# Optimization experiments

Measured on AMD Instinct MI355X. Metric: run time of the kernel, lower is better.

## Reference

```python
import jax, jax.numpy as jnp
import numpy as np

E, IN, OUT, T = 8, 4096, 4096, 8192
GS = IN  # groupsize=-1 -> groupsize = infeatures


def setup_inputs() -> dict:
    key = jax.random.key(0)
    k1, k2, k3, k4, k5 = jax.random.split(key, 5)
    x = jax.random.normal(k1, (T, IN), dtype=jnp.float16)
    indices = jax.random.randint(k2, (T,), 0, E, dtype=jnp.int32)
    # int32 words each packing 8 int4 nonzero values (2:4 sparse -> IN*OUT/2 values per expert)
    qweight = jax.random.randint(k3, (E, IN // 32, OUT * 16 // 8), 0, 2**31 - 1, dtype=jnp.int32)
    meta = jax.random.randint(k4, (E, OUT, IN // 16), 0, 2**15, dtype=jnp.int32).astype(jnp.int16)
    scales = (jax.random.uniform(k5, (E, IN // GS, OUT), dtype=jnp.float32) * 0.02 + 0.001).astype(jnp.float16)
    return {"x": x, "indices": indices, "qweight": qweight, "meta": meta, "scales": scales}


def _dequant_24(qweight, meta, scales):
    """Decode packed int4 + 2:4-sparsity metadata into dense fp32 weights (E, OUT, IN)."""
    # unpack 8 int4 nibbles per int32 word, symmetric zero-point 8
    nib = (qweight[..., None] >> (4 * jnp.arange(8, dtype=jnp.int32))) & 0xF  # (E, IN//32, 2*OUT, 8)
    vals = nib.reshape(E, IN // 2, OUT).transpose(0, 2, 1).astype(jnp.float32) - 8.0  # (E, OUT, IN//2)
    m = meta.astype(jnp.int32) & 0xFFFF
    sub = (m[..., None] >> (2 * jnp.arange(8, dtype=jnp.int32))) & 0x3  # (E, OUT, IN//16, 8)
    grp = (jnp.arange(8, dtype=jnp.int32) // 2) * 4                      # group-of-4 base within 16-block
    base = 16 * jnp.arange(IN // 16, dtype=jnp.int32)                    # 16-block base
    dense_col = (base[None, None, :, None] + grp[None, None, None, :] + sub).reshape(E, OUT, IN // 2)
    eidx = jnp.arange(E)[:, None, None]
    oidx = jnp.arange(OUT)[None, :, None]
    W = jnp.zeros((E, OUT, IN), jnp.float32).at[eidx, oidx, dense_col].add(vals)
    # per-group dequant scales: (E, IN//GS, OUT) -> (E, OUT, IN)
    s = jnp.repeat(scales.astype(jnp.float32), GS, axis=1).transpose(0, 2, 1)
    return W * s


def reference(x, indices, qweight, meta, scales):
    W = _dequant_24(qweight, meta, scales)  # (E, OUT, IN)
    y = jnp.zeros((x.shape[0], OUT), jnp.float32)
    for e in range(E):  # fixed small expert count
        xe = jnp.where((indices == e)[:, None], x, 0).astype(jnp.float32)
        y = y + xe @ W[e].T
    return y.astype(x.dtype)
```

## Files before the change

kernel.cpp:

```cpp
#include <hip/hip_runtime.h>

#define E_N   8
#define IN_N  4096
#define OUT_N 4096
#define T_N   8192

#define BM 128
#define BN 256
#define BK 64
#define NTHREADS 512

typedef unsigned short u16;
typedef __bf16 bf16_t;
typedef bf16_t bf16x8 __attribute__((ext_vector_type(8)));
typedef u16    u16x8  __attribute__((ext_vector_type(8)));
typedef float  f32x4  __attribute__((ext_vector_type(4)));

#define GLOAD16(gsrc, ldst) \
    __builtin_amdgcn_global_load_lds( \
        (const __attribute__((address_space(1))) unsigned int*)(gsrc), \
        (__attribute__((address_space(3))) unsigned int*)(ldst), 16, 0, 0)

__device__ int g_cnt[E_N];
__device__ int g_base[E_N];
__device__ int g_ids[T_N];
__device__ int g_meta_wide;
__device__ u16 g_W[(long)E_N * OUT_N * IN_N];
__device__ u16 g_xb[(long)T_N * IN_N];

__device__ __forceinline__ u16 f2bf(float f) {
    unsigned u = __builtin_bit_cast(unsigned, f);
    u += 0x7FFFu + ((u >> 16) & 1u);
    return (u16)(u >> 16);
}

__global__ void sort_tokens(const int* __restrict__ idx, const u16* __restrict__ meta16) {
    __shared__ int cnt[E_N], off[E_N];
    __shared__ int probe;
    const int tid = threadIdx.x;
    if (tid == 0) probe = 0;
    if (tid < E_N) cnt[tid] = 0;
    __syncthreads();
    if (tid < 64) {
        unsigned v = meta16[2 * (tid * 131072) + 1];
        if (v) atomicOr(&probe, 1);
    }
    for (int t = tid; t < T_N; t += blockDim.x) atomicAdd(&cnt[idx[t] & 7], 1);
    __syncthreads();
    if (tid == 0) {
        int s = 0;
        for (int e = 0; e < E_N; ++e) { g_cnt[e] = cnt[e]; g_base[e] = s; off[e] = s; s += cnt[e]; }
        g_meta_wide = (probe == 0) ? 1 : 0;
    }
    __syncthreads();
    for (int t = tid; t < T_N; t += blockDim.x) {
        int p = atomicAdd(&off[idx[t] & 7], 1);
        if (p >= 0 && p < T_N) g_ids[p] = t;
    }
}

__global__ __launch_bounds__(256, 4)
void xb_convert(const float* __restrict__ x) {
    const int p = blockIdx.x;
    int tok = g_ids[p];
    if ((unsigned)tok >= (unsigned)T_N) tok = 0;
    const float* src = x + (long)tok * IN_N;
    u16* dst = g_xb + (long)p * IN_N;
    const int tid = threadIdx.x;
    float va[16];
    #pragma unroll
    for (int c4 = 0; c4 < 4; ++c4) {
        float4 v = *reinterpret_cast<const float4*>(src + tid * 16 + c4 * 4);
        va[c4 * 4 + 0] = v.x; va[c4 * 4 + 1] = v.y; va[c4 * 4 + 2] = v.z; va[c4 * 4 + 3] = v.w;
    }
    unsigned wp[8];
    #pragma unroll
    for (int p8 = 0; p8 < 8; ++p8)
        wp[p8] = (unsigned)f2bf(va[2 * p8]) | ((unsigned)f2bf(va[2 * p8 + 1]) << 16);
    *reinterpret_cast<int4*>(dst + tid * 16)     = make_int4((int)wp[0], (int)wp[1], (int)wp[2], (int)wp[3]);
    *reinterpret_cast<int4*>(dst + tid * 16 + 8) = make_int4((int)wp[4], (int)wp[5], (int)wp[6], (int)wp[7]);
}

__global__ __launch_bounds__(256, 4)
void decode_w(const int* __restrict__ qw, const void* __restrict__ meta) {
    const int e   = blockIdx.z;
    const int kt0 = blockIdx.y * 4;
    const int o   = blockIdx.x * 256 + threadIdx.x;
    const bool mwide = (g_meta_wide != 0);
    unsigned mws[16];
    if (mwide) {
        const int* mp = (const int*)meta + ((long)e * OUT_N + o) * (IN_N / 16) + kt0 * 4;
        #pragma unroll
        for (int i = 0; i < 16; ++i) mws[i] = (unsigned)mp[i] & 0xFFFFu;
    } else {
        const u16* mp = (const u16*)meta + ((long)e * OUT_N + o) * (IN_N / 16) + kt0 * 4;
        #pragma unroll
        for (int i = 0; i < 16; ++i) mws[i] = mp[i];
    }
    const unsigned sh = (o & 7) << 2;
    #pragma unroll
    for (int ki = 0; ki < 4; ++ki) {
        const int kt = kt0 + ki;
        unsigned wp[32];
        #pragma unroll
        for (int gi = 0; gi < 4; ++gi) {
            const int g = kt * 4 + gi;
            const unsigned mw = mws[ki * 4 + gi];
            const int* qp = qw + ((e * (IN_N / 32) + (g >> 1)) << 13) + (o >> 3) + ((g & 1) << 12);
            int d[16];
            #pragma unroll
            for (int p = 0; p < 16; ++p) d[p] = 0;
            #pragma unroll
            for (int grp = 0; grp < 4; ++grp) {
                const unsigned w0 = (unsigned)qp[(2 * grp) * 512];
                const unsigned w1 = (unsigned)qp[(2 * grp + 1) * 512];
                const int v0 = (int)((w0 >> sh) & 0xF) - 8;
                const int v1 = (int)((w1 >> sh) & 0xF) - 8;
                const int s0 = (mw >> (4 * grp)) & 3;
                const int s1 = (mw >> (4 * grp + 2)) & 3;
                #pragma unroll
                for (int q = 0; q < 4; ++q) {
                    int t0 = (s0 == q) ? v0 : 0;
                    int t1 = (s1 == q) ? v1 : 0;
                    d[grp * 4 + q] = t0 + t1;
                }
            }
            #pragma unroll
            for (int p = 0; p < 8; ++p) {
                unsigned lo = __builtin_bit_cast(unsigned, (float)d[2 * p])     >> 16;
                unsigned hi = __builtin_bit_cast(unsigned, (float)d[2 * p + 1]) >> 16;
                wp[gi * 8 + p] = lo | (hi << 16);
            }
        }
        u16* wr = g_W + ((long)(e * 64 + kt) * OUT_N + o) * 64;
        #pragma unroll
        for (int q4 = 0; q4 < 8; ++q4)
            *reinterpret_cast<int4*>(wr + q4 * 8) =
                make_int4((int)wp[q4 * 4], (int)wp[q4 * 4 + 1], (int)wp[q4 * 4 + 2], (int)wp[q4 * 4 + 3]);
    }
}

__global__ __launch_bounds__(NTHREADS, 1)
void moe_gemm(const float* __restrict__ scales, float* __restrict__ y) {
    const int e = blockIdx.z;
    int cnt = g_cnt[e];
    if (cnt < 0) cnt = 0;
    if (cnt > T_N) cnt = T_N;
    const int m0 = blockIdx.y * BM;
    if (m0 >= cnt) return;
    const int n0 = blockIdx.x * BN;
    int base = g_base[e];
    if (base < 0) base = 0;
    if (base > T_N - cnt) base = T_N - cnt;

    __shared__ __align__(16) u16 As[BM * BK];
    __shared__ __align__(16) u16 Bs[BN * BK];

    const int tid  = threadIdx.x;
    const int lane = tid & 63;
    const int wm   = (tid >> 6) >> 2;
    const int wn   = (tid >> 6) & 3;

    const int r0 = tid >> 3, kc = tid & 7;
    long ar0 = (long)base + m0 + r0;       if (ar0 > T_N - 1) ar0 = T_N - 1;
    long ar1 = (long)base + m0 + 64 + r0;  if (ar1 > T_N - 1) ar1 = T_N - 1;
    const u16* asrc0 = g_xb + ar0 * IN_N + kc * 8;
    const u16* asrc1 = g_xb + ar1 * IN_N + kc * 8;
    u16* adst0 = &As[tid * 8];
    u16* adst1 = &As[(tid + 512) * 8];
    const u16* bsrc = g_W + ((long)e * 64 * OUT_N + n0) * 64 + tid * 8;

    f32x4 acc[4][4];
    #pragma unroll
    for (int i = 0; i < 4; ++i)
        #pragma unroll
        for (int j = 0; j < 4; ++j) acc[i][j] = (f32x4){0.f, 0.f, 0.f, 0.f};

    for (int k0 = 0; k0 < IN_N; k0 += BK) {
        GLOAD16(asrc0 + k0, adst0);
        GLOAD16(asrc1 + k0, adst1);
        #pragma unroll
        for (int it = 0; it < 4; ++it)
            GLOAD16(bsrc + it * 4096, &Bs[(tid + it * 512) * 8]);
        bsrc += (long)OUT_N * 64;
        __syncthreads();
        #pragma unroll
        for (int kk = 0; kk < BK; kk += 32) {
            bf16x8 af[4], bfr[4];
            #pragma unroll
            for (int mf = 0; mf < 4; ++mf) {
                const int r = wm * 64 + mf * 16 + (lane & 15);
                u16x8 v = *reinterpret_cast<const u16x8*>(&As[r * 64 + kk + ((lane >> 4) << 3)]);
                af[mf] = __builtin_bit_cast(bf16x8, v);
            }
            #pragma unroll
            for (int nf = 0; nf < 4; ++nf) {
                const int r = wn * 64 + nf * 16 + (lane & 15);
                u16x8 v = *reinterpret_cast<const u16x8*>(&Bs[r * 64 + kk + ((lane >> 4) << 3)]);
                bfr[nf] = __builtin_bit_cast(bf16x8, v);
            }
            #pragma unroll
            for (int mf = 0; mf < 4; ++mf)
                #pragma unroll
                for (int nf = 0; nf < 4; ++nf)
                    acc[mf][nf] = __builtin_amdgcn_mfma_f32_16x16x32_bf16(af[mf], bfr[nf], acc[mf][nf], 0, 0, 0);
        }
        __syncthreads();
    }

    const int* toks = g_ids + base;
    float sc[4];
    #pragma unroll
    for (int nf = 0; nf < 4; ++nf)
        sc[nf] = scales[e * OUT_N + n0 + wn * 64 + nf * 16 + (lane & 15)];
    #pragma unroll
    for (int mf = 0; mf < 4; ++mf) {
        #pragma unroll
        for (int r = 0; r < 4; ++r) {
            const int row = m0 + wm * 64 + mf * 16 + ((lane >> 4) << 2) + r;
            if (row >= cnt) continue;
            int tok = toks[row];
            if ((unsigned)tok >= (unsigned)T_N) continue;
            float* yrow = y + (long)tok * OUT_N;
            #pragma unroll
            for (int nf = 0; nf < 4; ++nf) {
                const int col = n0 + wn * 64 + nf * 16 + (lane & 15);
                yrow[col] = acc[mf][nf][r] * sc[nf];
            }
        }
    }
}

extern "C" void kernel_launch(void* const* d_in, const int* in_sizes, int n_in,
                              void* d_out, int out_size, void* d_ws, size_t ws_size,
                              hipStream_t stream) {
    const float* x      = nullptr;
    const int* indices  = nullptr;
    const int* qw       = nullptr;
    const void* meta    = nullptr;
    const float* scales = nullptr;
    int big_seen = 0;
    for (int i = 0; i < n_in; ++i) {
        long s = in_sizes[i];
        if (s == 33554432L)      x = (const float*)d_in[i];
        else if (s == 8192L)     indices = (const int*)d_in[i];
        else if (s == 32768L)    scales = (const float*)d_in[i];
        else if (s == 8388608L) {
            if (big_seen++ == 0)  qw = (const int*)d_in[i];
            else                  meta = d_in[i];
        }
    }
    if (!x || !indices || !qw || !meta || !scales) return;
    float* y = (float*)d_out;

    hipLaunchKernelGGL(sort_tokens, dim3(1), dim3(1024), 0, stream, indices, (const u16*)meta);
    hipLaunchKernelGGL(xb_convert, dim3(T_N), dim3(256), 0, stream, x);
    hipLaunchKernelGGL(decode_w, dim3(OUT_N / 256, 16, E_N), dim3(256), 0, stream, qw, meta);
    hipLaunchKernelGGL(moe_gemm, dim3(OUT_N / BN, T_N / BM, E_N), dim3(NTHREADS), 0, stream, scales, y);
}
```

Before: 725.5 us.

## XOR-swizzle LDS tiles to remove bank conflicts; warp-aggregate token sort atomics

The A tile load now fetches 16-byte chunks from a column chosen by XORing with the row, so the LDS layout is swizzled. The decoded weight matrix is written to global memory in the same XOR-permuted chunk order, which lets the B tile keep its straight copy. The fragment reads apply the matching XOR, which should remove LDS bank conflicts on the row-strided 128-byte reads. Separately, the token sort replaces per-thread shared atomics with ballot/popcount warp aggregation, trading more instructions for fewer atomics in a tiny kernel.

```diff
diff --git a/kernel.cpp b/kernel.cpp
--- a/kernel.cpp
+++ b/kernel.cpp
@@ -38,6 +38,7 @@
     __shared__ int cnt[E_N], off[E_N];
     __shared__ int probe;
     const int tid = threadIdx.x;
+    const int lane = tid & 63;
     if (tid == 0) probe = 0;
     if (tid < E_N) cnt[tid] = 0;
     __syncthreads();
@@ -45,7 +46,15 @@
         unsigned v = meta16[2 * (tid * 131072) + 1];
         if (v) atomicOr(&probe, 1);
     }
-    for (int t = tid; t < T_N; t += blockDim.x) atomicAdd(&cnt[idx[t] & 7], 1);
+    for (int t0 = tid - lane; t0 < T_N; t0 += blockDim.x) {
+        const int t = t0 + lane;
+        const int my = idx[t] & 7;
+        #pragma unroll
+        for (int e = 0; e < E_N; ++e) {
+            unsigned long long m = __ballot(my == e);
+            if (lane == 0 && m) atomicAdd(&cnt[e], __popcll(m));
+        }
+    }
     __syncthreads();
     if (tid == 0) {
         int s = 0;
@@ -53,9 +62,22 @@
         g_meta_wide = (probe == 0) ? 1 : 0;
     }
     __syncthreads();
-    for (int t = tid; t < T_N; t += blockDim.x) {
-        int p = atomicAdd(&off[idx[t] & 7], 1);
-        if (p >= 0 && p < T_N) g_ids[p] = t;
+    for (int t0 = tid - lane; t0 < T_N; t0 += blockDim.x) {
+        const int t = t0 + lane;
+        const int my = idx[t] & 7;
+        #pragma unroll
+        for (int e = 0; e < E_N; ++e) {
+            unsigned long long m = __ballot(my == e);
+            if (my == e) {
+                int below = __popcll(m & ((1ull << lane) - 1ull));
+                int basep = 0;
+                if (below == 0) basep = atomicAdd(&off[e], __popcll(m));
+                int src = __ffsll((long long)m) - 1;
+                basep = __shfl(basep, src);
+                int p = basep + below;
+                if (p >= 0 && p < T_N) g_ids[p] = t;
+            }
+        }
     }
 }
 
@@ -98,6 +120,7 @@
         for (int i = 0; i < 16; ++i) mws[i] = mp[i];
     }
     const unsigned sh = (o & 7) << 2;
+    const int osw = o & 7;
     #pragma unroll
     for (int ki = 0; ki < 4; ++ki) {
         const int kt = kt0 + ki;
@@ -134,9 +157,9 @@
         }
         u16* wr = g_W + ((long)(e * 64 + kt) * OUT_N + o) * 64;
         #pragma unroll
-        for (int q4 = 0; q4 < 8; ++q4)
-            *reinterpret_cast<int4*>(wr + q4 * 8) =
-                make_int4((int)wp[q4 * 4], (int)wp[q4 * 4 + 1], (int)wp[q4 * 4 + 2], (int)wp[q4 * 4 + 3]);
+        for (int h = 0; h < 8; ++h)
+            *reinterpret_cast<int4*>(wr + (h ^ osw) * 8) =
+                make_int4((int)wp[h * 4], (int)wp[h * 4 + 1], (int)wp[h * 4 + 2], (int)wp[h * 4 + 3]);
     }
 }
 
@@ -161,11 +184,12 @@
     const int wm   = (tid >> 6) >> 2;
     const int wn   = (tid >> 6) & 3;
 
-    const int r0 = tid >> 3, kc = tid & 7;
+    const int r0 = tid >> 3;
+    const int kc_swz = (tid & 7) ^ (r0 & 7);
     long ar0 = (long)base + m0 + r0;       if (ar0 > T_N - 1) ar0 = T_N - 1;
     long ar1 = (long)base + m0 + 64 + r0;  if (ar1 > T_N - 1) ar1 = T_N - 1;
-    const u16* asrc0 = g_xb + ar0 * IN_N + kc * 8;
-    const u16* asrc1 = g_xb + ar1 * IN_N + kc * 8;
+    const u16* asrc0 = g_xb + ar0 * IN_N + kc_swz * 8;
+    const u16* asrc1 = g_xb + ar1 * IN_N + kc_swz * 8;
     u16* adst0 = &As[tid * 8];
     u16* adst1 = &As[(tid + 512) * 8];
     const u16* bsrc = g_W + ((long)e * 64 * OUT_N + n0) * 64 + tid * 8;
@@ -190,13 +214,15 @@
             #pragma unroll
             for (int mf = 0; mf < 4; ++mf) {
                 const int r = wm * 64 + mf * 16 + (lane & 15);
-                u16x8 v = *reinterpret_cast<const u16x8*>(&As[r * 64 + kk + ((lane >> 4) << 3)]);
+                const int h = (kk >> 3) + (lane >> 4);
+                u16x8 v = *reinterpret_cast<const u16x8*>(&As[r * 64 + ((h ^ (r & 7)) << 3)]);
                 af[mf] = __builtin_bit_cast(bf16x8, v);
             }
             #pragma unroll
             for (int nf = 0; nf < 4; ++nf) {
                 const int r = wn * 64 + nf * 16 + (lane & 15);
-                u16x8 v = *reinterpret_cast<const u16x8*>(&Bs[r * 64 + kk + ((lane >> 4) << 3)]);
+                const int h = (kk >> 3) + (lane >> 4);
+                u16x8 v = *reinterpret_cast<const u16x8*>(&Bs[r * 64 + ((h ^ (r & 7)) << 3)]);
                 bfr[nf] = __builtin_bit_cast(bf16x8, v);
             }
             #pragma unroll
```

After: 653.8 us. 9.9% less time.
